# Performance work log

Measured on AMD Instinct MI355X. Metric: run time of the kernel, lower is better.

The kernel has to match this reference:

```python
import jax, jax.numpy as jnp
import numpy as np

N_NODES = 65536
N_PER = 1024      # nodes per graph
NUM_GRAPHS = 64
N_EDGES = 1048576
IN_DIM = 192
PE_DIM = 64
HIDDEN = 256
LATENT = 128
POOL_RATIO = 0.5
K_PER = int(np.ceil(POOL_RATIO * N_PER))  # 512 kept per graph


def setup_inputs() -> dict:
    key = jax.random.key(0)
    ks = jax.random.split(key, 12)
    x_raw = jax.random.normal(ks[0], (N_NODES, IN_DIM), dtype=jnp.float32)
    sincos_pe = jax.random.normal(ks[1], (N_NODES, PE_DIM), dtype=jnp.float32)
    edge_index = jax.random.randint(ks[2], (2, N_EDGES), 0, N_NODES, dtype=jnp.int64)
    batch = (jnp.arange(N_NODES, dtype=jnp.int64) // N_PER)
    eps = jax.random.normal(ks[3], (N_NODES, LATENT), dtype=jnp.float32)
    # learned parameters (GCNConv: Linear no-bias weight + separate bias; TopKPooling weight)
    def glorot(k, shape):
        lim = float(np.sqrt(6.0 / (shape[0] + shape[1])))
        return jax.random.uniform(k, shape, jnp.float32, -lim, lim)
    W1 = glorot(ks[4], (IN_DIM + PE_DIM, HIDDEN))
    b1 = jnp.zeros((HIDDEN,), jnp.float32)
    Wmu = glorot(ks[5], (HIDDEN, LATENT))
    bmu = jnp.zeros((LATENT,), jnp.float32)
    Wlv = glorot(ks[6], (HIDDEN, LATENT))
    blv = jnp.zeros((LATENT,), jnp.float32)
    w_pool = jax.random.uniform(ks[7], (LATENT,), jnp.float32, -1.0, 1.0) / np.sqrt(LATENT)
    return {"x_raw": x_raw, "sincos_pe": sincos_pe, "edge_index": edge_index,
            "batch": batch, "eps": eps, "W1": W1, "b1": b1, "Wmu": Wmu,
            "bmu": bmu, "Wlv": Wlv, "blv": blv, "w_pool": w_pool}


def _gcn_conv(x, W, b, src, dst, n):
    # PyG GCNConv: x' = D^{-1/2}(A+I)D^{-1/2} (x W) + b, self-loops already in src/dst
    h = x @ W                                   # [N, out]
    deg = jnp.zeros((n,), h.dtype).at[dst].add(1.0)
    dinv = jax.lax.rsqrt(deg)                   # deg >= 1 thanks to self-loops
    norm = dinv[src] * dinv[dst]                # [E+N]
    msg = norm[:, None] * h[src]                # gather (irregular)
    return jax.ops.segment_sum(msg, dst, num_segments=n) + b


def reference(x_raw, sincos_pe, edge_index, batch, eps, W1, b1, Wmu, bmu, Wlv, blv, w_pool):
    n = x_raw.shape[0]
    loops = jnp.arange(n, dtype=edge_index.dtype)
    src = jnp.concatenate([edge_index[0], loops])
    dst = jnp.concatenate([edge_index[1], loops])

    x_in = jnp.concatenate([x_raw, sincos_pe], axis=-1)
    h = jax.nn.relu(_gcn_conv(x_in, W1, b1, src, dst, n))
    mu = _gcn_conv(h, Wmu, bmu, src, dst, n)
    logvar = _gcn_conv(h, Wlv, blv, src, dst, n)
    z = mu + eps * jnp.exp(0.5 * logvar)

    # TopKPooling: score = tanh((z . w)/||w||); keep top ratio per graph
    score = jnp.tanh((z @ w_pool) / jnp.linalg.norm(w_pool))   # [N]
    s2 = score.reshape(NUM_GRAPHS, N_PER)
    _, idx = jax.lax.top_k(s2, K_PER)                           # descending per graph
    perm = (idx + (jnp.arange(NUM_GRAPHS) * N_PER)[:, None]).reshape(-1)
    z_pool = z[perm] * score[perm][:, None]
    mu_pool = mu[perm]
    logvar_pool = logvar[perm]
    batch_pool = batch[perm]
    return z_pool, mu_pool, logvar_pool, batch_pool, perm
```

## Files before the change

kernel.cpp:

```cpp
#include <hip/hip_runtime.h>
#include <hip/hip_fp16.h>
#include <math.h>

#define NN      65536
#define NE      1048576
#define NPER    1024
#define NGRAPH  64
#define KPER    512
#define IND     192
#define PED     64
#define HID     256
#define LAT     128

#define OFF_CNT     0u
#define OFF_ROWPTR  65536u
#define OFF_CUR     132096u
#define OFF_DINV    198656u
#define OFF_EPK     264192u
#define OFF_INVWN   2361344u
#define OFF_KEEP    2361360u
#define OFF_SCORE   2395136u
#define OFF_WT1     2460672u
#define OFF_WT2     2493440u
#define OFF_T0B     2526208u
#define OFF_HB      6720512u
#define OFF_MUB     6720512u
#define OFF_LVB     10914816u

#define OUT_MU      4194304
#define OUT_LV      8388608
#define OUT_BATCH   12582912
#define OUT_PERM    12615680

typedef __attribute__((ext_vector_type(8))) short short8;
typedef __attribute__((ext_vector_type(4))) float floatx4;

__device__ __forceinline__ unsigned short f2bf(float f) {
    unsigned int u = __float_as_uint(f);
    u += 0x7FFFu + ((u >> 16) & 1u);
    return (unsigned short)(u >> 16);
}
__device__ __forceinline__ float bf2f(unsigned short u) {
    return __uint_as_float(((unsigned int)u) << 16);
}
__device__ __forceinline__ unsigned int pack2bf(float x, float y) {
    const unsigned int ux = __float_as_uint(x) + 0x8000u;
    const unsigned int uy = __float_as_uint(y) + 0x8000u;
    return __builtin_amdgcn_perm(uy, ux, 0x07060302u);
}
__device__ __forceinline__ unsigned char f2e5(float f) {
    unsigned short u = __half_as_ushort(__float2half(f));
    u += (unsigned short)(0x7Fu + ((u >> 8) & 1u));
    return (unsigned char)(u >> 8);
}
__device__ __forceinline__ void store_bf8x4(unsigned char* base, float v0, float v1, float v2, float v3) {
#if __has_builtin(__builtin_amdgcn_cvt_pk_bf8_f32)
    const unsigned int r01 = (unsigned int)__builtin_amdgcn_cvt_pk_bf8_f32(v0, v1, 0, false);
    const unsigned int r23 = (unsigned int)__builtin_amdgcn_cvt_pk_bf8_f32(v2, v3, 0, false);
    base[0]   = (unsigned char)r01;
    base[256] = (unsigned char)(r01 >> 8);
    base[512] = (unsigned char)r23;
    base[768] = (unsigned char)(r23 >> 8);
#else
    base[0] = f2e5(v0); base[256] = f2e5(v1); base[512] = f2e5(v2); base[768] = f2e5(v3);
#endif
}
__device__ __forceinline__ __half2 e5lo(unsigned int u) {
    return __builtin_bit_cast(__half2, __builtin_amdgcn_perm(u, 0u, 0x05000400u));
}
__device__ __forceinline__ __half2 e5hi(unsigned int u) {
    return __builtin_bit_cast(__half2, __builtin_amdgcn_perm(u, 0u, 0x07000600u));
}

__global__ __launch_bounds__(256) void k_count(const int* __restrict__ ei, int* __restrict__ cnt) {
    int e = blockIdx.x * 256 + threadIdx.x;
    atomicAdd(&cnt[ei[NE + e]], 1);
}

__global__ __launch_bounds__(1024) void k_scan(const int* __restrict__ cnt, int* __restrict__ rp,
                                               float* __restrict__ dinv) {
    __shared__ int part[1024];
    const int t = threadIdx.x;
    const int base = t * 64;
    int loc[64];
#pragma unroll
    for (int i = 0; i < 64; i += 4)
        *(int4*)&loc[i] = *(const int4*)(cnt + base + i);
    int s = 0;
#pragma unroll
    for (int i = 0; i < 64; ++i) s += loc[i];
    part[t] = s;
    __syncthreads();
    for (int d = 1; d < 1024; d <<= 1) {
        int v = (t >= d) ? part[t - d] : 0;
        __syncthreads();
        part[t] += v;
        __syncthreads();
    }
    int run = part[t] - s;
    int rpo[64];
    float dv[64];
#pragma unroll
    for (int i = 0; i < 64; ++i) {
        rpo[i] = run;
        run += loc[i];
        dv[i] = 1.0f / sqrtf((float)(loc[i] + 1));
    }
#pragma unroll
    for (int i = 0; i < 64; i += 4) {
        *(int4*)(rp + base + i) = *(int4*)&rpo[i];
        *(float4*)(dinv + base + i) = *(float4*)&dv[i];
    }
    if (t == 1023) rp[NN] = run;
}

__global__ __launch_bounds__(256) void k_scatter(const int* __restrict__ ei, const int* __restrict__ rp,
                                                 int* __restrict__ cur, const float* __restrict__ dinv,
                                                 int2* __restrict__ epk) {
    int e = blockIdx.x * 256 + threadIdx.x;
    int s = ei[e];
    int d = ei[NE + e];
    int pos = rp[d] + atomicAdd(&cur[d], 1);
    epk[pos] = make_int2(s, __float_as_int(dinv[s] * dinv[d]));
}

__global__ __launch_bounds__(128) void k_wnorm(const float* __restrict__ wp, float* __restrict__ invwn) {
    __shared__ float red[128];
    int t = threadIdx.x;
    float v = wp[t];
    red[t] = v * v;
    __syncthreads();
    for (int s = 64; s > 0; s >>= 1) {
        if (t < s) red[t] += red[t + s];
        __syncthreads();
    }
    if (t == 0) invwn[0] = 1.0f / sqrtf(red[0]);
}

__global__ __launch_bounds__(256) void k_prepw(const float* __restrict__ W1, const float* __restrict__ Wmu,
                                               const float* __restrict__ Wlv, unsigned short* __restrict__ wt1,
                                               unsigned short* __restrict__ wt2) {
    const int n = blockIdx.x, k = threadIdx.x;
    wt1[n * 256 + k] = f2bf(W1[k * 256 + n]);
    wt2[n * 256 + k] = f2bf((n < 128) ? Wmu[k * 128 + n] : Wlv[k * 128 + (n - 128)]);
}

template <int MODE>
__global__ __launch_bounds__(256, 2) void k_gemm(const float* __restrict__ A0f, const float* __restrict__ A1f,
                                                 const unsigned short* __restrict__ Ah,
                                                 const unsigned short* __restrict__ Wt,
                                                 unsigned char* __restrict__ Cb) {
    __shared__ unsigned short lds[2][12288];
    const int tid = threadIdx.x;
    const int w = __builtin_amdgcn_readfirstlane(tid >> 6);
    const int lane = tid & 63;
    const int l = lane & 15, q = lane >> 4;
    const int Rbase = blockIdx.x * 128;

    const int rs = tid >> 1;
    const int ch = tid & 1;
    const int stile = rs >> 4, sl = rs & 15, q0 = ch * 2;
    const int uA = (stile * 4 + q0) * 16 + sl;

    floatx4 acc[16][2];
#pragma unroll
    for (int nt = 0; nt < 16; ++nt) {
        acc[nt][0] = (floatx4)0.0f;
        acc[nt][1] = (floatx4)0.0f;
    }

    auto stage = [&](int ks, int buf) {
        if (MODE == 0) {
            const float* p; int ld, col;
            const int k = ks * 32 + ch * 16;
            if (ks < 6) { p = A0f; ld = IND; col = k; }
            else        { p = A1f; ld = PED; col = k - IND; }
            const float* src = p + (size_t)(Rbase + rs) * ld + col;
            unsigned int pk[8];
#pragma unroll
            for (int j = 0; j < 16; j += 4) {
                const float4 t = *(const float4*)(src + j);
                pk[j / 2]     = pack2bf(t.x, t.y);
                pk[j / 2 + 1] = pack2bf(t.z, t.w);
            }
            *(uint4*)&lds[buf][uA * 8]        = *(uint4*)&pk[0];
            *(uint4*)&lds[buf][(uA + 16) * 8] = *(uint4*)&pk[4];
        } else {
            const unsigned short* src = Ah + (size_t)(Rbase + rs) * 256 + ks * 32 + ch * 16;
            *(uint4*)&lds[buf][uA * 8]        = ((const uint4*)src)[0];
            *(uint4*)&lds[buf][(uA + 16) * 8] = ((const uint4*)src)[1];
        }
#pragma unroll
        for (int rep = 0; rep < 2; ++rep) {
            const int n = rep * 128 + rs;
            const unsigned short* srcB = Wt + (size_t)n * 256 + ks * 32 + ch * 16;
            const uint4 w0 = ((const uint4*)srcB)[0];
            const uint4 w1 = ((const uint4*)srcB)[1];
            const int uB = ((n >> 4) * 4 + q0) * 16 + (n & 15);
            *(uint4*)&lds[buf][4096 + uB * 8]        = w0;
            *(uint4*)&lds[buf][4096 + (uB + 16) * 8] = w1;
        }
    };

    stage(0, 0);
    __syncthreads();
#pragma unroll
    for (int ks = 0; ks < 8; ++ks) {
        const int cur = ks & 1;
        if (ks < 7) stage(ks + 1, cur ^ 1);
        const short8 a0 = *(const short8*)&lds[cur][(((2 * w) * 4 + q) * 16 + l) * 8];
        const short8 a1 = *(const short8*)&lds[cur][(((2 * w + 1) * 4 + q) * 16 + l) * 8];
#pragma unroll
        for (int nt = 0; nt < 16; ++nt) {
            const short8 b = *(const short8*)&lds[cur][4096 + ((nt * 4 + q) * 16 + l) * 8];
            acc[nt][0] = __builtin_amdgcn_mfma_f32_16x16x32_bf16(a0, b, acc[nt][0], 0, 0, 0);
            acc[nt][1] = __builtin_amdgcn_mfma_f32_16x16x32_bf16(a1, b, acc[nt][1], 0, 0, 0);
        }
        if (ks < 7) __syncthreads();
    }

#pragma unroll
    for (int m = 0; m < 2; ++m) {
        const int mt = 2 * w + m;
#pragma unroll
        for (int nt = 0; nt < 16; ++nt) {
            const floatx4 v = acc[nt][m];
            unsigned char* base = Cb + (size_t)(Rbase + mt * 16 + q * 4) * 256 + nt * 16 + l;
            store_bf8x4(base, v[0], v[1], v[2], v[3]);
        }
    }
}

template <int PHASE>
__global__ __launch_bounds__(256) void k_agg(const unsigned char* __restrict__ tb, const int* __restrict__ rp,
                                             const int2* __restrict__ epk, const float* __restrict__ dinv,
                                             const float* __restrict__ bias0, const float* __restrict__ bias1,
                                             const float* __restrict__ eps, const float* __restrict__ wp,
                                             const float* __restrict__ invwn, unsigned short* __restrict__ hb,
                                             unsigned short* __restrict__ mub, unsigned short* __restrict__ lvb,
                                             float* __restrict__ score) {
    const int wv = __builtin_amdgcn_readfirstlane(threadIdx.x >> 6);
    const int lane = threadIdx.x & 63;
    const int node = blockIdx.x * 4 + wv;
    const int c0 = lane * 4;
    const float di = dinv[node];
    const unsigned char* tbc = tb + c0;

    const unsigned int vs = *(const unsigned int*)(tbc + ((size_t)node << 8));
    const __half2 ws2 = __float2half2_rn(di * di);
    __half2 a01 = __hmul2(ws2, e5lo(vs));
    __half2 a23 = __hmul2(ws2, e5hi(vs));
    __half2 b01 = __float2half2_rn(0.0f);
    __half2 b23 = __float2half2_rn(0.0f);

    const int beg = rp[node], end = rp[node + 1];
    int p = beg;
    if (p + 8 <= end) {
        int2 e0 = epk[p],     e1 = epk[p + 1], e2 = epk[p + 2], e3 = epk[p + 3];
        int2 e4 = epk[p + 4], e5 = epk[p + 5], e6 = epk[p + 6], e7 = epk[p + 7];
        for (;;) {
            const int2 f0 = epk[p + 8],  f1 = epk[p + 9],  f2 = epk[p + 10], f3 = epk[p + 11];
            const int2 f4 = epk[p + 12], f5 = epk[p + 13], f6 = epk[p + 14], f7 = epk[p + 15];
            const unsigned int v0 = *(const unsigned int*)(tbc + ((size_t)__builtin_amdgcn_readfirstlane(e0.x) << 8));
            const unsigned int v1 = *(const unsigned int*)(tbc + ((size_t)__builtin_amdgcn_readfirstlane(e1.x) << 8));
            const unsigned int v2 = *(const unsigned int*)(tbc + ((size_t)__builtin_amdgcn_readfirstlane(e2.x) << 8));
            const unsigned int v3 = *(const unsigned int*)(tbc + ((size_t)__builtin_amdgcn_readfirstlane(e3.x) << 8));
            const unsigned int v4 = *(const unsigned int*)(tbc + ((size_t)__builtin_amdgcn_readfirstlane(e4.x) << 8));
            const unsigned int v5 = *(const unsigned int*)(tbc + ((size_t)__builtin_amdgcn_readfirstlane(e5.x) << 8));
            const unsigned int v6 = *(const unsigned int*)(tbc + ((size_t)__builtin_amdgcn_readfirstlane(e6.x) << 8));
            const unsigned int v7 = *(const unsigned int*)(tbc + ((size_t)__builtin_amdgcn_readfirstlane(e7.x) << 8));
            const __half2 w0 = __float2half2_rn(__int_as_float(e0.y));
            const __half2 w1 = __float2half2_rn(__int_as_float(e1.y));
            const __half2 w2 = __float2half2_rn(__int_as_float(e2.y));
            const __half2 w3 = __float2half2_rn(__int_as_float(e3.y));
            const __half2 w4 = __float2half2_rn(__int_as_float(e4.y));
            const __half2 w5 = __float2half2_rn(__int_as_float(e5.y));
            const __half2 w6 = __float2half2_rn(__int_as_float(e6.y));
            const __half2 w7 = __float2half2_rn(__int_as_float(e7.y));
            a01 = __hfma2(w0, e5lo(v0), a01); a23 = __hfma2(w0, e5hi(v0), a23);
            b01 = __hfma2(w1, e5lo(v1), b01); b23 = __hfma2(w1, e5hi(v1), b23);
            a01 = __hfma2(w2, e5lo(v2), a01); a23 = __hfma2(w2, e5hi(v2), a23);
            b01 = __hfma2(w3, e5lo(v3), b01); b23 = __hfma2(w3, e5hi(v3), b23);
            a01 = __hfma2(w4, e5lo(v4), a01); a23 = __hfma2(w4, e5hi(v4), a23);
            b01 = __hfma2(w5, e5lo(v5), b01); b23 = __hfma2(w5, e5hi(v5), b23);
            a01 = __hfma2(w6, e5lo(v6), a01); a23 = __hfma2(w6, e5hi(v6), a23);
            b01 = __hfma2(w7, e5lo(v7), b01); b23 = __hfma2(w7, e5hi(v7), b23);
            p += 8;
            if (p + 8 > end) break;
            e0 = f0; e1 = f1; e2 = f2; e3 = f3;
            e4 = f4; e5 = f5; e6 = f6; e7 = f7;
        }
    }
    if (p + 4 <= end) {
        const int2 e0 = epk[p], e1 = epk[p + 1], e2 = epk[p + 2], e3 = epk[p + 3];
        const unsigned int v0 = *(const unsigned int*)(tbc + ((size_t)__builtin_amdgcn_readfirstlane(e0.x) << 8));
        const unsigned int v1 = *(const unsigned int*)(tbc + ((size_t)__builtin_amdgcn_readfirstlane(e1.x) << 8));
        const unsigned int v2 = *(const unsigned int*)(tbc + ((size_t)__builtin_amdgcn_readfirstlane(e2.x) << 8));
        const unsigned int v3 = *(const unsigned int*)(tbc + ((size_t)__builtin_amdgcn_readfirstlane(e3.x) << 8));
        const __half2 w0 = __float2half2_rn(__int_as_float(e0.y));
        const __half2 w1 = __float2half2_rn(__int_as_float(e1.y));
        const __half2 w2 = __float2half2_rn(__int_as_float(e2.y));
        const __half2 w3 = __float2half2_rn(__int_as_float(e3.y));
        a01 = __hfma2(w0, e5lo(v0), a01); a23 = __hfma2(w0, e5hi(v0), a23);
        b01 = __hfma2(w1, e5lo(v1), b01); b23 = __hfma2(w1, e5hi(v1), b23);
        a01 = __hfma2(w2, e5lo(v2), a01); a23 = __hfma2(w2, e5hi(v2), a23);
        b01 = __hfma2(w3, e5lo(v3), b01); b23 = __hfma2(w3, e5hi(v3), b23);
        p += 4;
    }
    for (; p < end; ++p) {
        const int2 e = epk[p];
        const unsigned int v = *(const unsigned int*)(tbc + ((size_t)__builtin_amdgcn_readfirstlane(e.x) << 8));
        const __half2 w2 = __float2half2_rn(__int_as_float(e.y));
        a01 = __hfma2(w2, e5lo(v), a01);
        a23 = __hfma2(w2, e5hi(v), a23);
    }
    a01 = __hadd2(a01, b01);
    a23 = __hadd2(a23, b23);
    const float2 flo = __half22float2(a01);
    const float2 fhi = __half22float2(a23);
    float4 acc = make_float4(flo.x, flo.y, fhi.x, fhi.y);

    if (PHASE == 0) {
        const float4 bb = *(const float4*)(bias0 + c0);
        ushort4 r;
        r.x = f2bf(fmaxf(acc.x + bb.x, 0.0f));
        r.y = f2bf(fmaxf(acc.y + bb.y, 0.0f));
        r.z = f2bf(fmaxf(acc.z + bb.z, 0.0f));
        r.w = f2bf(fmaxf(acc.w + bb.w, 0.0f));
        *(ushort4*)(hb + ((size_t)node << 8) + c0) = r;
    } else {
        const int cb = (lane & 31) * 4;
        const float* bias = (lane < 32) ? bias0 : bias1;
        const float4 bb = *(const float4*)(bias + cb);
        acc.x += bb.x; acc.y += bb.y; acc.z += bb.z; acc.w += bb.w;
        unsigned short* dst = (lane < 32) ? mub : lvb;
        ushort4 st;
        st.x = f2bf(acc.x); st.y = f2bf(acc.y); st.z = f2bf(acc.z); st.w = f2bf(acc.w);
        *(ushort4*)(dst + (size_t)node * 128 + cb) = st;
        float4 l4;
        l4.x = __shfl(acc.x, lane | 32, 64);
        l4.y = __shfl(acc.y, lane | 32, 64);
        l4.z = __shfl(acc.z, lane | 32, 64);
        l4.w = __shfl(acc.w, lane | 32, 64);
        float partial = 0.0f;
        if (lane < 32) {
            const float4 e4 = *(const float4*)(eps + (size_t)node * 128 + cb);
            const float4 w4 = *(const float4*)(wp + cb);
            float zx = fmaf(e4.x, expf(0.5f * l4.x), acc.x);
            float zy = fmaf(e4.y, expf(0.5f * l4.y), acc.y);
            float zz = fmaf(e4.z, expf(0.5f * l4.z), acc.z);
            float zw = fmaf(e4.w, expf(0.5f * l4.w), acc.w);
            partial = zx * w4.x + zy * w4.y + zz * w4.z + zw * w4.w;
        }
        for (int off = 16; off > 0; off >>= 1) partial += __shfl_xor(partial, off, 64);
        if (lane == 0) score[node] = tanhf(partial * invwn[0]);
    }
}

__global__ __launch_bounds__(512) void k_topk(const float* __restrict__ score, const int* __restrict__ batch,
                                              int* __restrict__ keep, float* __restrict__ out) {
    __shared__ float sk[1024];
    __shared__ int si[1024];
    const int g = blockIdx.x, t = threadIdx.x;
    for (int i = t; i < 1024; i += 512) {
        sk[i] = score[g * 1024 + i];
        si[i] = i;
    }
    __syncthreads();
    for (int k = 2; k <= 1024; k <<= 1) {
        for (int j = k >> 1; j > 0; j >>= 1) {
            for (int base = 0; base < 1024; base += 512) {
                int i = base + t;
                int ixj = i ^ j;
                if (ixj > i) {
                    float a = sk[i], b = sk[ixj];
                    int ia = si[i], ib = si[ixj];
                    bool before = (a > b) || (a == b && ia < ib);
                    bool up = ((i & k) == 0);
                    bool sw = up ? (!before) : before;
                    if (sw) {
                        sk[i] = b; si[i] = ib;
                        sk[ixj] = a; si[ixj] = ia;
                    }
                }
            }
            __syncthreads();
        }
    }
    if (t < KPER) {
        int node = g * 1024 + si[t];
        keep[g * KPER + t] = node;
        out[OUT_BATCH + g * KPER + t] = (float)batch[node];
        out[OUT_PERM + g * KPER + t] = (float)node;
    }
}

__global__ __launch_bounds__(128) void k_gather(const int* __restrict__ keep,
                                                const unsigned short* __restrict__ mub,
                                                const unsigned short* __restrict__ lvb,
                                                const float* __restrict__ eps,
                                                const float* __restrict__ score, float* __restrict__ out) {
    const int kidx = blockIdx.x;
    const int c = threadIdx.x;
    const int node = keep[kidx];
    const float m = bf2f(mub[(size_t)node * 128 + c]);
    const float l = bf2f(lvb[(size_t)node * 128 + c]);
    const float e = eps[(size_t)node * 128 + c];
    const float z = fmaf(e, expf(0.5f * l), m);
    const float s = score[node];
    out[(size_t)kidx * 128 + c] = z * s;
    out[OUT_MU + (size_t)kidx * 128 + c] = m;
    out[OUT_LV + (size_t)kidx * 128 + c] = l;
}

extern "C" void kernel_launch(void* const* d_in, const int* in_sizes, int n_in,
                              void* d_out, int out_size, void* d_ws, size_t ws_size,
                              hipStream_t stream) {
    (void)in_sizes; (void)n_in; (void)out_size; (void)ws_size;
    const float* x_raw = (const float*)d_in[0];
    const float* pe    = (const float*)d_in[1];
    const int*   ei    = (const int*)d_in[2];
    const int*   batch = (const int*)d_in[3];
    const float* eps   = (const float*)d_in[4];
    const float* W1    = (const float*)d_in[5];
    const float* b1    = (const float*)d_in[6];
    const float* Wmu   = (const float*)d_in[7];
    const float* bmu   = (const float*)d_in[8];
    const float* Wlv   = (const float*)d_in[9];
    const float* blv   = (const float*)d_in[10];
    const float* wp    = (const float*)d_in[11];
    float* ws = (float*)d_ws;
    int*  iws = (int*)d_ws;
    int2* epk = (int2*)(iws + OFF_EPK);
    unsigned short* wt1  = (unsigned short*)(ws + OFF_WT1);
    unsigned short* wt2  = (unsigned short*)(ws + OFF_WT2);
    unsigned char*  t0b  = (unsigned char*)(ws + OFF_T0B);
    unsigned short* hb16 = (unsigned short*)(ws + OFF_HB);
    unsigned short* mub  = (unsigned short*)(ws + OFF_MUB);
    unsigned short* lvb  = (unsigned short*)(ws + OFF_LVB);
    float* out = (float*)d_out;

    hipMemsetAsync(iws + OFF_CNT, 0, 65536 * 4, stream);
    hipMemsetAsync(iws + OFF_CUR, 0, 65536 * 4, stream);

    k_count<<<NE / 256, 256, 0, stream>>>(ei, iws + OFF_CNT);
    k_scan<<<1, 1024, 0, stream>>>(iws + OFF_CNT, iws + OFF_ROWPTR, ws + OFF_DINV);
    k_scatter<<<NE / 256, 256, 0, stream>>>(ei, iws + OFF_ROWPTR, iws + OFF_CUR, ws + OFF_DINV, epk);
    k_wnorm<<<1, 128, 0, stream>>>(wp, ws + OFF_INVWN);
    k_prepw<<<256, 256, 0, stream>>>(W1, Wmu, Wlv, wt1, wt2);

    k_gemm<0><<<NN / 128, 256, 0, stream>>>(x_raw, pe, nullptr, wt1, t0b);
    k_agg<0><<<NN / 4, 256, 0, stream>>>(t0b, iws + OFF_ROWPTR, epk, ws + OFF_DINV,
                                         b1, nullptr, nullptr, nullptr, nullptr,
                                         hb16, nullptr, nullptr, nullptr);
    k_gemm<1><<<NN / 128, 256, 0, stream>>>(nullptr, nullptr, hb16, wt2, t0b);
    k_agg<1><<<NN / 4, 256, 0, stream>>>(t0b, iws + OFF_ROWPTR, epk, ws + OFF_DINV,
                                         bmu, blv, eps, wp, ws + OFF_INVWN,
                                         nullptr, mub, lvb, ws + OFF_SCORE);
    k_topk<<<NGRAPH, 512, 0, stream>>>(ws + OFF_SCORE, batch, iws + OFF_KEEP, out);
    k_gather<<<NGRAPH * KPER, 128, 0, stream>>>(iws + OFF_KEEP, mub, lvb, eps,
                                                ws + OFF_SCORE, out);
}
```

Before: 442.4 us.

## Retile GEMM warps to 4x8 MFMA blocks and software-pipeline aggregation gathers

The GEMM now gives each wave a 4-row by 8-column tile block instead of 2 rows by all 16 columns. That lowers LDS B-fragment reads per MFMA at the cost of more A loads. The aggregation loop is restructured so the feature gathers for the next group of 8 edges are issued before the FMAs of the current group, and edge metadata is prefetched two groups ahead. This is meant to hide gather latency, at the cost of more live registers. In the aggregation loop, epk is read up to 16 entries past the current position, which may read beyond a node's edge range. It can also read past the end of the array unless padding exists.

```diff
diff --git a/kernel.cpp b/kernel.cpp
--- a/kernel.cpp
+++ b/kernel.cpp
@@ -156,18 +156,19 @@
     const int lane = tid & 63;
     const int l = lane & 15, q = lane >> 4;
     const int Rbase = blockIdx.x * 128;
+    const int mtb = (w >> 1) * 4;
+    const int ntb = (w & 1) * 8;
 
     const int rs = tid >> 1;
     const int ch = tid & 1;
     const int stile = rs >> 4, sl = rs & 15, q0 = ch * 2;
     const int uA = (stile * 4 + q0) * 16 + sl;
 
-    floatx4 acc[16][2];
-#pragma unroll
-    for (int nt = 0; nt < 16; ++nt) {
-        acc[nt][0] = (floatx4)0.0f;
-        acc[nt][1] = (floatx4)0.0f;
-    }
+    floatx4 acc[8][4];
+#pragma unroll
+    for (int j = 0; j < 8; ++j)
+#pragma unroll
+        for (int m = 0; m < 4; ++m) acc[j][m] = (floatx4)0.0f;
 
     auto stage = [&](int ks, int buf) {
         if (MODE == 0) {
@@ -208,27 +209,35 @@
     for (int ks = 0; ks < 8; ++ks) {
         const int cur = ks & 1;
         if (ks < 7) stage(ks + 1, cur ^ 1);
-        const short8 a0 = *(const short8*)&lds[cur][(((2 * w) * 4 + q) * 16 + l) * 8];
-        const short8 a1 = *(const short8*)&lds[cur][(((2 * w + 1) * 4 + q) * 16 + l) * 8];
-#pragma unroll
-        for (int nt = 0; nt < 16; ++nt) {
-            const short8 b = *(const short8*)&lds[cur][4096 + ((nt * 4 + q) * 16 + l) * 8];
-            acc[nt][0] = __builtin_amdgcn_mfma_f32_16x16x32_bf16(a0, b, acc[nt][0], 0, 0, 0);
-            acc[nt][1] = __builtin_amdgcn_mfma_f32_16x16x32_bf16(a1, b, acc[nt][1], 0, 0, 0);
+        short8 a[4];
+#pragma unroll
+        for (int m = 0; m < 4; ++m)
+            a[m] = *(const short8*)&lds[cur][(((mtb + m) * 4 + q) * 16 + l) * 8];
+#pragma unroll
+        for (int j = 0; j < 8; ++j) {
+            const short8 b = *(const short8*)&lds[cur][4096 + (((ntb + j) * 4 + q) * 16 + l) * 8];
+#pragma unroll
+            for (int m = 0; m < 4; ++m)
+                acc[j][m] = __builtin_amdgcn_mfma_f32_16x16x32_bf16(a[m], b, acc[j][m], 0, 0, 0);
         }
         if (ks < 7) __syncthreads();
     }
 
 #pragma unroll
-    for (int m = 0; m < 2; ++m) {
-        const int mt = 2 * w + m;
-#pragma unroll
-        for (int nt = 0; nt < 16; ++nt) {
-            const floatx4 v = acc[nt][m];
+    for (int m = 0; m < 4; ++m) {
+        const int mt = mtb + m;
+#pragma unroll
+        for (int j = 0; j < 8; ++j) {
+            const int nt = ntb + j;
+            const floatx4 v = acc[j][m];
             unsigned char* base = Cb + (size_t)(Rbase + mt * 16 + q * 4) * 256 + nt * 16 + l;
             store_bf8x4(base, v[0], v[1], v[2], v[3]);
         }
     }
+}
+
+__device__ __forceinline__ unsigned int gath(const unsigned char* tbc, int srcv) {
+    return *(const unsigned int*)(tbc + ((size_t)__builtin_amdgcn_readfirstlane(srcv) << 8));
 }
 
 template <int PHASE>
@@ -256,47 +265,47 @@
     const int beg = rp[node], end = rp[node + 1];
     int p = beg;
     if (p + 8 <= end) {
-        int2 e0 = epk[p],     e1 = epk[p + 1], e2 = epk[p + 2], e3 = epk[p + 3];
-        int2 e4 = epk[p + 4], e5 = epk[p + 5], e6 = epk[p + 6], e7 = epk[p + 7];
-        for (;;) {
-            const int2 f0 = epk[p + 8],  f1 = epk[p + 9],  f2 = epk[p + 10], f3 = epk[p + 11];
-            const int2 f4 = epk[p + 12], f5 = epk[p + 13], f6 = epk[p + 14], f7 = epk[p + 15];
-            const unsigned int v0 = *(const unsigned int*)(tbc + ((size_t)__builtin_amdgcn_readfirstlane(e0.x) << 8));
-            const unsigned int v1 = *(const unsigned int*)(tbc + ((size_t)__builtin_amdgcn_readfirstlane(e1.x) << 8));
-            const unsigned int v2 = *(const unsigned int*)(tbc + ((size_t)__builtin_amdgcn_readfirstlane(e2.x) << 8));
-            const unsigned int v3 = *(const unsigned int*)(tbc + ((size_t)__builtin_amdgcn_readfirstlane(e3.x) << 8));
-            const unsigned int v4 = *(const unsigned int*)(tbc + ((size_t)__builtin_amdgcn_readfirstlane(e4.x) << 8));
-            const unsigned int v5 = *(const unsigned int*)(tbc + ((size_t)__builtin_amdgcn_readfirstlane(e5.x) << 8));
-            const unsigned int v6 = *(const unsigned int*)(tbc + ((size_t)__builtin_amdgcn_readfirstlane(e6.x) << 8));
-            const unsigned int v7 = *(const unsigned int*)(tbc + ((size_t)__builtin_amdgcn_readfirstlane(e7.x) << 8));
-            const __half2 w0 = __float2half2_rn(__int_as_float(e0.y));
-            const __half2 w1 = __float2half2_rn(__int_as_float(e1.y));
-            const __half2 w2 = __float2half2_rn(__int_as_float(e2.y));
-            const __half2 w3 = __float2half2_rn(__int_as_float(e3.y));
-            const __half2 w4 = __float2half2_rn(__int_as_float(e4.y));
-            const __half2 w5 = __float2half2_rn(__int_as_float(e5.y));
-            const __half2 w6 = __float2half2_rn(__int_as_float(e6.y));
-            const __half2 w7 = __float2half2_rn(__int_as_float(e7.y));
-            a01 = __hfma2(w0, e5lo(v0), a01); a23 = __hfma2(w0, e5hi(v0), a23);
-            b01 = __hfma2(w1, e5lo(v1), b01); b23 = __hfma2(w1, e5hi(v1), b23);
-            a01 = __hfma2(w2, e5lo(v2), a01); a23 = __hfma2(w2, e5hi(v2), a23);
-            b01 = __hfma2(w3, e5lo(v3), b01); b23 = __hfma2(w3, e5hi(v3), b23);
-            a01 = __hfma2(w4, e5lo(v4), a01); a23 = __hfma2(w4, e5hi(v4), a23);
-            b01 = __hfma2(w5, e5lo(v5), b01); b23 = __hfma2(w5, e5hi(v5), b23);
-            a01 = __hfma2(w6, e5lo(v6), a01); a23 = __hfma2(w6, e5hi(v6), a23);
-            b01 = __hfma2(w7, e5lo(v7), b01); b23 = __hfma2(w7, e5hi(v7), b23);
+        int2 em[8], en[8];
+        unsigned int v[8];
+#pragma unroll
+        for (int i = 0; i < 8; ++i) em[i] = epk[p + i];
+#pragma unroll
+        for (int i = 0; i < 8; ++i) v[i] = gath(tbc, em[i].x);
+#pragma unroll
+        for (int i = 0; i < 8; ++i) en[i] = epk[p + 8 + i];
+        while (p + 16 <= end) {
+            int2 ef[8];
+#pragma unroll
+            for (int i = 0; i < 8; ++i) ef[i] = epk[p + 16 + i];
+            unsigned int u[8];
+#pragma unroll
+            for (int i = 0; i < 8; ++i) u[i] = gath(tbc, en[i].x);
+#pragma unroll
+            for (int i = 0; i < 8; i += 2) {
+                const __half2 wA = __float2half2_rn(__int_as_float(em[i].y));
+                const __half2 wB = __float2half2_rn(__int_as_float(em[i + 1].y));
+                a01 = __hfma2(wA, e5lo(v[i]), a01);     a23 = __hfma2(wA, e5hi(v[i]), a23);
+                b01 = __hfma2(wB, e5lo(v[i + 1]), b01); b23 = __hfma2(wB, e5hi(v[i + 1]), b23);
+            }
+#pragma unroll
+            for (int i = 0; i < 8; ++i) { em[i] = en[i]; en[i] = ef[i]; v[i] = u[i]; }
             p += 8;
-            if (p + 8 > end) break;
-            e0 = f0; e1 = f1; e2 = f2; e3 = f3;
-            e4 = f4; e5 = f5; e6 = f6; e7 = f7;
-        }
+        }
+#pragma unroll
+        for (int i = 0; i < 8; i += 2) {
+            const __half2 wA = __float2half2_rn(__int_as_float(em[i].y));
+            const __half2 wB = __float2half2_rn(__int_as_float(em[i + 1].y));
+            a01 = __hfma2(wA, e5lo(v[i]), a01);     a23 = __hfma2(wA, e5hi(v[i]), a23);
+            b01 = __hfma2(wB, e5lo(v[i + 1]), b01); b23 = __hfma2(wB, e5hi(v[i + 1]), b23);
+        }
+        p += 8;
     }
     if (p + 4 <= end) {
         const int2 e0 = epk[p], e1 = epk[p + 1], e2 = epk[p + 2], e3 = epk[p + 3];
-        const unsigned int v0 = *(const unsigned int*)(tbc + ((size_t)__builtin_amdgcn_readfirstlane(e0.x) << 8));
-        const unsigned int v1 = *(const unsigned int*)(tbc + ((size_t)__builtin_amdgcn_readfirstlane(e1.x) << 8));
-        const unsigned int v2 = *(const unsigned int*)(tbc + ((size_t)__builtin_amdgcn_readfirstlane(e2.x) << 8));
-        const unsigned int v3 = *(const unsigned int*)(tbc + ((size_t)__builtin_amdgcn_readfirstlane(e3.x) << 8));
+        const unsigned int v0 = gath(tbc, e0.x);
+        const unsigned int v1 = gath(tbc, e1.x);
+        const unsigned int v2 = gath(tbc, e2.x);
+        const unsigned int v3 = gath(tbc, e3.x);
         const __half2 w0 = __float2half2_rn(__int_as_float(e0.y));
         const __half2 w1 = __float2half2_rn(__int_as_float(e1.y));
         const __half2 w2 = __float2half2_rn(__int_as_float(e2.y));
@@ -309,7 +318,7 @@
     }
     for (; p < end; ++p) {
         const int2 e = epk[p];
-        const unsigned int v = *(const unsigned int*)(tbc + ((size_t)__builtin_amdgcn_readfirstlane(e.x) << 8));
+        const unsigned int v = gath(tbc, e.x);
         const __half2 w2 = __float2half2_rn(__int_as_float(e.y));
         a01 = __hfma2(w2, e5lo(v), a01);
         a23 = __hfma2(w2, e5hi(v), a23);
```

Result: no change. 439.9 us (-0.6%).
